# Optimization experiments

Hardware: AMD Instinct MI355X
Metric: run time of the kernel (lower is better)

## Reference

```python
import jax, jax.numpy as jnp
import numpy as np

B, L_IN, D = 4, 4096, 1024
R_MIN, R_MAX = 0.9, 0.999


def setup_inputs() -> dict:
    key = jax.random.key(0)
    k0, k1, k2 = jax.random.split(key, 3)
    inputs = jax.random.normal(k0, (B, L_IN, D), jnp.float32)
    Wi = jax.random.normal(k1, (2 * D, D), jnp.float32) / np.sqrt(D)
    bi = jnp.zeros((2 * D,), jnp.float32)
    Wo = jax.random.normal(k2, (D, 2 * D), jnp.float32) / np.sqrt(2 * D)
    bo = jnp.zeros((D,), jnp.float32)
    # LRU stable-ring initialization, exactly as in the torch module
    rng = np.random.default_rng(0)
    u1 = rng.random(D)
    u2 = rng.random(D)
    v_log = np.log(-0.5 * np.log(u1 * (R_MAX ** 2 - R_MIN ** 2) + R_MIN ** 2))
    theta_log = np.log(u2 * np.pi * 2)
    gamma_log = np.log(np.sqrt(1.0 - np.exp(-np.exp(v_log)) ** 2))
    params_log = jnp.asarray(np.stack([v_log, theta_log, gamma_log]), jnp.float32)
    return {"inputs": inputs, "Wi": Wi, "bi": bi, "Wo": Wo, "bo": bo,
            "params_log": params_log}


def _lru_forward(inputs, Wi, bi, Wo, bo, params_log):
    b, l_in, d = inputs.shape
    u = inputs @ Wi.T + bi                      # [B, L, 2D]
    v, theta, gamma = jnp.exp(params_log)       # each [D]
    # torch.view_as_complex: interleaved (real, imag) pairs along last dim
    uc = u.reshape(b, l_in, d, 2)
    x = jax.lax.complex(uc[..., 0], uc[..., 1])  # [B, L, D] complex64
    log2_L = int(np.ceil(np.log2(l_in)))
    L = 2 ** log2_L
    x = jnp.pad(x, ((0, 0), (0, L - l_in), (0, 0)))
    # Blelloch-style log-depth scan: x_t = lambda * x_{t-1} + u_t,
    # lambda = exp(-v + i*theta)
    for i in range(1, log2_L + 1):
        blk = 2 ** i
        xb = x.reshape(b * L // blk, blk, d)
        x1, x2 = xb[:, : blk // 2], xb[:, blk // 2:]
        pos = jnp.arange(1, blk // 2 + 1, dtype=jnp.float32)  # [blk/2]
        lambs = jnp.exp(jax.lax.complex(-pos[:, None] * v,
                                        pos[:, None] * theta))  # [blk/2, D]
        x2 = x2 + lambs * x1[:, -1:]
        x = jnp.concatenate([x1, x2], axis=1).reshape(b, L, d)
    x = x[:, :l_in] * gamma.astype(x.dtype)     # normalize, drop padding
    xr = jnp.concatenate([x.real, x.imag], axis=-1)  # [B, L, 2D]
    out = xr @ Wo.T + bo
    return jax.nn.relu(out)


def reference(inputs, Wi, bi, Wo, bo, params_log):
    return _lru_forward(inputs, Wi, bi, Wo, bo, params_log)
```

## Files before the change

### kernel.cpp

```cpp
#include <hip/hip_runtime.h>

#define BB 4
#define LL 4096
#define DD 1024
#define SS 64
#define TT 64

typedef __attribute__((ext_vector_type(16))) float  floatx16;
typedef __attribute__((ext_vector_type(8)))  short  shortx8;

static __device__ __forceinline__ unsigned short f2bf(float f) {
    unsigned int u = __float_as_uint(f);
    u += 0x7fffu + ((u >> 16) & 1u);
    return (unsigned short)(u >> 16);
}
static __device__ __forceinline__ float bf2f(unsigned short h) {
    return __uint_as_float(((unsigned int)h) << 16);
}

#define NIN4 (BB * LL * DD / 4)
#define NW4  (2 * DD * DD / 4)
__global__ void cast_all_kernel(const float4* __restrict__ s_in, ushort4* __restrict__ d_inb,
                                const float4* __restrict__ s_wi, ushort4* __restrict__ d_wib,
                                const float4* __restrict__ s_wo, ushort4* __restrict__ d_wob) {
    int i = blockIdx.x * blockDim.x + threadIdx.x;
    const float4* s; ushort4* d; int j;
    if (i < NIN4)                 { s = s_in; d = d_inb; j = i; }
    else if (i < NIN4 + NW4)      { s = s_wi; d = d_wib; j = i - NIN4; }
    else                          { s = s_wo; d = d_wob; j = i - NIN4 - NW4; }
    float4 v = s[j];
    ushort4 o;
    o.x = f2bf(v.x); o.y = f2bf(v.y); o.z = f2bf(v.z); o.w = f2bf(v.w);
    d[j] = o;
}

template<int K, int NT, int EPI>
__global__ __launch_bounds__(256)
void gemm_bt(const unsigned short* __restrict__ A,
             const unsigned short* __restrict__ B,
             const float* __restrict__ bias,
             void* __restrict__ Cp) {
    constexpr int N = NT * 128;
    __shared__ __align__(16) short As[128 * 32];
    __shared__ __align__(16) short Bs[128 * 32];

    const int tid = threadIdx.x;
    const int b   = blockIdx.x;
    const int xcd = b & 7;
    const int i2  = b >> 3;
    const int tileM = ((i2 / NT) * 8 + xcd) * 128;
    const int tileN = (i2 % NT) * 128;

    const int lane = tid & 63;
    const int wave = tid >> 6;
    const int wm   = (wave >> 1) * 64;
    const int wn   = (wave & 1) * 64;
    const int r32  = lane & 31;
    const int ks   = lane >> 5;

    floatx16 acc[2][2] = {};

    const int q0 = tid, q1 = tid + 256;
    const int ra0 = q0 >> 2, ca0 = ((q0 & 3) ^ ((ra0 >> 1) & 3)) * 8;
    const int ra1 = q1 >> 2, ca1 = ((q1 & 3) ^ ((ra1 >> 1) & 3)) * 8;
    short* As0 = &As[(q0 & ~63) * 8];
    short* As1 = &As[(q1 & ~63) * 8];
    short* Bs0 = &Bs[(q0 & ~63) * 8];
    short* Bs1 = &Bs[(q1 & ~63) * 8];

    for (int k0 = 0; k0 < K; k0 += 32) {
        __builtin_amdgcn_global_load_lds(
            (const __attribute__((address_space(1))) void*)&A[(size_t)(tileM + ra0) * K + k0 + ca0],
            (__attribute__((address_space(3))) void*)As0, 16, 0, 0);
        __builtin_amdgcn_global_load_lds(
            (const __attribute__((address_space(1))) void*)&A[(size_t)(tileM + ra1) * K + k0 + ca1],
            (__attribute__((address_space(3))) void*)As1, 16, 0, 0);
        __builtin_amdgcn_global_load_lds(
            (const __attribute__((address_space(1))) void*)&B[(size_t)(tileN + ra0) * K + k0 + ca0],
            (__attribute__((address_space(3))) void*)Bs0, 16, 0, 0);
        __builtin_amdgcn_global_load_lds(
            (const __attribute__((address_space(1))) void*)&B[(size_t)(tileN + ra1) * K + k0 + ca1],
            (__attribute__((address_space(3))) void*)Bs1, 16, 0, 0);
        __syncthreads();

        shortx8 af[2][2], bfr[2][2];
#pragma unroll
        for (int i = 0; i < 2; ++i) {
            const int row = wm + i * 32 + r32;
            const int sw  = (row >> 1) & 3;
#pragma unroll
            for (int kc = 0; kc < 2; ++kc)
                af[i][kc] = *(const shortx8*)(&As[row * 32 + ((kc * 2 + ks) ^ sw) * 8]);
        }
#pragma unroll
        for (int j = 0; j < 2; ++j) {
            const int row = wn + j * 32 + r32;
            const int sw  = (row >> 1) & 3;
#pragma unroll
            for (int kc = 0; kc < 2; ++kc)
                bfr[j][kc] = *(const shortx8*)(&Bs[row * 32 + ((kc * 2 + ks) ^ sw) * 8]);
        }
#pragma unroll
        for (int kc = 0; kc < 2; ++kc)
#pragma unroll
            for (int i = 0; i < 2; ++i)
#pragma unroll
                for (int j = 0; j < 2; ++j)
                    acc[i][j] = __builtin_amdgcn_mfma_f32_32x32x16_bf16(
                        af[i][kc], bfr[j][kc], acc[i][j], 0, 0, 0);
        __syncthreads();
    }

#pragma unroll
    for (int i = 0; i < 2; ++i) {
#pragma unroll
        for (int j = 0; j < 2; ++j) {
            const int col = tileN + wn + j * 32 + r32;
            const float bv = bias[col];
#pragma unroll
            for (int r = 0; r < 16; ++r) {
                const int row = tileM + wm + i * 32 + (r & 3) + 8 * (r >> 2) + 4 * ks;
                float v = acc[i][j][r] + bv;
                if (EPI == 0) {
                    ((unsigned short*)Cp)[(size_t)row * N + col] = f2bf(v);
                } else {
                    ((float*)Cp)[(size_t)row * N + col] = fmaxf(v, 0.0f);
                }
            }
        }
    }
}

__global__ __launch_bounds__(256)
void scanA(const unsigned short* __restrict__ u,
           const float* __restrict__ plog,
           float2* __restrict__ Eend) {
    const int d0 = (blockIdx.x * 256 + threadIdx.x) * 2;
    const int c = blockIdx.y, b = blockIdx.z;
    const float v0  = expf(plog[d0]),      v1  = expf(plog[d0 + 1]);
    const float th0 = expf(plog[DD + d0]), th1 = expf(plog[DD + d0 + 1]);
    const float a0 = expf(-v0), a1 = expf(-v1);
    const float lr0 = a0 * cosf(th0), li0 = a0 * sinf(th0);
    const float lr1 = a1 * cosf(th1), li1 = a1 * sinf(th1);
    float zr0 = 0.f, zi0 = 0.f, zr1 = 0.f, zi1 = 0.f;
    const unsigned short* up = u + (size_t)(b * LL + c * TT) * (2 * DD) + 2 * d0;
#pragma unroll 4
    for (int tl = 0; tl < TT; ++tl) {
        uint2 pr = *(const uint2*)up;
        float xr0 = bf2f((unsigned short)(pr.x & 0xffffu));
        float xi0 = bf2f((unsigned short)(pr.x >> 16));
        float xr1 = bf2f((unsigned short)(pr.y & 0xffffu));
        float xi1 = bf2f((unsigned short)(pr.y >> 16));
        float t;
        t = lr0 * zr0 - li0 * zi0 + xr0; zi0 = lr0 * zi0 + li0 * zr0 + xi0; zr0 = t;
        t = lr1 * zr1 - li1 * zi1 + xr1; zi1 = lr1 * zi1 + li1 * zr1 + xi1; zr1 = t;
        up += 2 * DD;
    }
    *(float4*)&Eend[(size_t)c * (BB * DD) + b * DD + d0] =
        make_float4(zr0, zi0, zr1, zi1);
}

__global__ __launch_bounds__(256)
void scanC(const unsigned short* __restrict__ u,
           const float* __restrict__ plog,
           const float2* __restrict__ Eend,
           unsigned short* __restrict__ xr) {
    const int d0 = (blockIdx.x * 256 + threadIdx.x) * 2;
    const int c = blockIdx.y, b = blockIdx.z;
    const float v0  = expf(plog[d0]),      v1  = expf(plog[d0 + 1]);
    const float th0 = expf(plog[DD + d0]), th1 = expf(plog[DD + d0 + 1]);
    const float g0  = expf(plog[2 * DD + d0]), g1 = expf(plog[2 * DD + d0 + 1]);
    const float a0 = expf(-v0), a1 = expf(-v1);
    const float lr0 = a0 * cosf(th0), li0 = a0 * sinf(th0);
    const float lr1 = a1 * cosf(th1), li1 = a1 * sinf(th1);

    const float aT0 = expf(-(float)TT * v0), aT1 = expf(-(float)TT * v1);
    const float Lr0 = aT0 * cosf((float)TT * th0), Li0 = aT0 * sinf((float)TT * th0);
    const float Lr1 = aT1 * cosf((float)TT * th1), Li1 = aT1 * sinf((float)TT * th1);
    float yr0 = 0.f, yi0 = 0.f, yr1 = 0.f, yi1 = 0.f;
    for (int cc = 0; cc < c; ++cc) {
        float4 e = *(const float4*)&Eend[(size_t)cc * (BB * DD) + b * DD + d0];
        float t;
        t = Lr0 * yr0 - Li0 * yi0 + e.x; yi0 = Lr0 * yi0 + Li0 * yr0 + e.y; yr0 = t;
        t = Lr1 * yr1 - Li1 * yi1 + e.z; yi1 = Lr1 * yi1 + Li1 * yr1 + e.w; yr1 = t;
    }

    const unsigned short* up = u + (size_t)(b * LL + c * TT) * (2 * DD) + 2 * d0;
    unsigned short* xp = xr + (size_t)(b * LL + c * TT) * (2 * DD) + d0;
#pragma unroll 4
    for (int tl = 0; tl < TT; ++tl) {
        uint2 pr = *(const uint2*)up;
        float xr0 = bf2f((unsigned short)(pr.x & 0xffffu));
        float xi0 = bf2f((unsigned short)(pr.x >> 16));
        float xr1 = bf2f((unsigned short)(pr.y & 0xffffu));
        float xi1 = bf2f((unsigned short)(pr.y >> 16));
        float t;
        t = lr0 * yr0 - li0 * yi0 + xr0; yi0 = lr0 * yi0 + li0 * yr0 + xi0; yr0 = t;
        t = lr1 * yr1 - li1 * yi1 + xr1; yi1 = lr1 * yi1 + li1 * yr1 + xi1; yr1 = t;
        *(unsigned int*)&xp[0]  = (unsigned int)f2bf(g0 * yr0) |
                                  ((unsigned int)f2bf(g1 * yr1) << 16);
        *(unsigned int*)&xp[DD] = (unsigned int)f2bf(g0 * yi0) |
                                  ((unsigned int)f2bf(g1 * yi1) << 16);
        up += 2 * DD;
        xp += 2 * DD;
    }
}

extern "C" void kernel_launch(void* const* d_in, const int* in_sizes, int n_in,
                              void* d_out, int out_size, void* d_ws, size_t ws_size,
                              hipStream_t stream) {
    const float* inputs = (const float*)d_in[0];
    const float* Wi     = (const float*)d_in[1];
    const float* bi     = (const float*)d_in[2];
    const float* Wo     = (const float*)d_in[3];
    const float* bo     = (const float*)d_in[4];
    const float* plog   = (const float*)d_in[5];
    float* out = (float*)d_out;

    const size_t M = (size_t)BB * LL;
    unsigned short* u_bf  = (unsigned short*)d_ws;
    unsigned short* xr_bf = u_bf  + M * 2 * DD;
    unsigned short* in_bf = xr_bf + M * 2 * DD;
    unsigned short* Wi_bf = in_bf + M * DD;
    unsigned short* Wo_bf = Wi_bf + (size_t)2 * DD * DD;
    float2* Eend = (float2*)(Wo_bf + (size_t)2 * DD * DD);

    {
        int total4 = NIN4 + 2 * NW4;
        cast_all_kernel<<<total4 / 256, 256, 0, stream>>>(
            (const float4*)inputs, (ushort4*)in_bf,
            (const float4*)Wi,     (ushort4*)Wi_bf,
            (const float4*)Wo,     (ushort4*)Wo_bf);
    }

    gemm_bt<DD, 16, 0><<<(M / 128) * 16, 256, 0, stream>>>(
        in_bf, Wi_bf, bi, (void*)u_bf);

    scanA<<<dim3(DD / 512, SS, BB), 256, 0, stream>>>(u_bf, plog, Eend);
    scanC<<<dim3(DD / 512, SS, BB), 256, 0, stream>>>(u_bf, plog, Eend, xr_bf);

    gemm_bt<2 * DD, 8, 1><<<(M / 128) * 8, 256, 0, stream>>>(
        xr_bf, Wo_bf, bo, (void*)out);
}
```

Before: 353.7 us.

## Switch GEMM to 16x16x32 MFMA with K-step 64 and 8-way swizzled LDS

The bf16 GEMM kernel now stages K=64 per iteration instead of 32, halving the number of barrier pairs per tile, and uses 16x16x32 MFMA instructions on a 4x4 grid of fragments per wave instead of 32x32x16 on a 2x2 grid. The LDS layout uses an 8-chunk XOR swizzle for the wider rows. This aims to cut synchronisation overhead and improve the load-to-compute ratio per step, in exchange for doubled LDS use per block and a different epilogue store pattern.

New measurement: 336.1 us. 5.0% less time.

```diff
diff --git a/kernel.cpp b/kernel.cpp
--- a/kernel.cpp
+++ b/kernel.cpp
@@ -6,8 +6,8 @@
 #define SS 64
 #define TT 64
 
-typedef __attribute__((ext_vector_type(16))) float  floatx16;
-typedef __attribute__((ext_vector_type(8)))  short  shortx8;
+typedef __attribute__((ext_vector_type(4))) float  floatx4;
+typedef __attribute__((ext_vector_type(8))) short  shortx8;
 
 static __device__ __forceinline__ unsigned short f2bf(float f) {
     unsigned int u = __float_as_uint(f);
@@ -41,8 +41,8 @@
              const float* __restrict__ bias,
              void* __restrict__ Cp) {
     constexpr int N = NT * 128;
-    __shared__ __align__(16) short As[128 * 32];
-    __shared__ __align__(16) short Bs[128 * 32];
+    __shared__ __align__(16) short As[128 * 64];
+    __shared__ __align__(16) short Bs[128 * 64];
 
     const int tid = threadIdx.x;
     const int b   = blockIdx.x;
@@ -51,75 +51,67 @@
     const int tileM = ((i2 / NT) * 8 + xcd) * 128;
     const int tileN = (i2 % NT) * 128;
 
-    const int lane = tid & 63;
-    const int wave = tid >> 6;
-    const int wm   = (wave >> 1) * 64;
-    const int wn   = (wave & 1) * 64;
-    const int r32  = lane & 31;
-    const int ks   = lane >> 5;
-
-    floatx16 acc[2][2] = {};
-
-    const int q0 = tid, q1 = tid + 256;
-    const int ra0 = q0 >> 2, ca0 = ((q0 & 3) ^ ((ra0 >> 1) & 3)) * 8;
-    const int ra1 = q1 >> 2, ca1 = ((q1 & 3) ^ ((ra1 >> 1) & 3)) * 8;
-    short* As0 = &As[(q0 & ~63) * 8];
-    short* As1 = &As[(q1 & ~63) * 8];
-    short* Bs0 = &Bs[(q0 & ~63) * 8];
-    short* Bs1 = &Bs[(q1 & ~63) * 8];
-
-    for (int k0 = 0; k0 < K; k0 += 32) {
-        __builtin_amdgcn_global_load_lds(
-            (const __attribute__((address_space(1))) void*)&A[(size_t)(tileM + ra0) * K + k0 + ca0],
-            (__attribute__((address_space(3))) void*)As0, 16, 0, 0);
-        __builtin_amdgcn_global_load_lds(
-            (const __attribute__((address_space(1))) void*)&A[(size_t)(tileM + ra1) * K + k0 + ca1],
-            (__attribute__((address_space(3))) void*)As1, 16, 0, 0);
-        __builtin_amdgcn_global_load_lds(
-            (const __attribute__((address_space(1))) void*)&B[(size_t)(tileN + ra0) * K + k0 + ca0],
-            (__attribute__((address_space(3))) void*)Bs0, 16, 0, 0);
-        __builtin_amdgcn_global_load_lds(
-            (const __attribute__((address_space(1))) void*)&B[(size_t)(tileN + ra1) * K + k0 + ca1],
-            (__attribute__((address_space(3))) void*)Bs1, 16, 0, 0);
+    const int lane  = tid & 63;
+    const int wave  = tid >> 6;
+    const int wm    = (wave >> 1) * 64;
+    const int wn    = (wave & 1) * 64;
+    const int r16   = lane & 15;
+    const int quad  = lane >> 4;
+
+    floatx4 acc[4][4] = {};
+
+    int rowS[4], colS[4];
+#pragma unroll
+    for (int n = 0; n < 4; ++n) {
+        const int q = tid + n * 256;
+        rowS[n] = q >> 3;
+        colS[n] = ((q & 7) ^ (rowS[n] & 7)) * 8;
+    }
+    const int ldsBase = (tid & ~63) * 8;
+
+    const int fx = r16 & 7;
+
+    for (int k0 = 0; k0 < K; k0 += 64) {
+#pragma unroll
+        for (int n = 0; n < 4; ++n) {
+            __builtin_amdgcn_global_load_lds(
+                (const __attribute__((address_space(1))) void*)&A[(size_t)(tileM + rowS[n]) * K + k0 + colS[n]],
+                (__attribute__((address_space(3))) void*)&As[ldsBase + n * 2048], 16, 0, 0);
+            __builtin_amdgcn_global_load_lds(
+                (const __attribute__((address_space(1))) void*)&B[(size_t)(tileN + rowS[n]) * K + k0 + colS[n]],
+                (__attribute__((address_space(3))) void*)&Bs[ldsBase + n * 2048], 16, 0, 0);
+        }
         __syncthreads();
 
-        shortx8 af[2][2], bfr[2][2];
-#pragma unroll
-        for (int i = 0; i < 2; ++i) {
-            const int row = wm + i * 32 + r32;
-            const int sw  = (row >> 1) & 3;
-#pragma unroll
-            for (int kc = 0; kc < 2; ++kc)
-                af[i][kc] = *(const shortx8*)(&As[row * 32 + ((kc * 2 + ks) ^ sw) * 8]);
+#pragma unroll
+        for (int kk = 0; kk < 2; ++kk) {
+            const int slot = ((kk * 4 + quad) ^ fx) * 8;
+            shortx8 af[4], bfv[4];
+#pragma unroll
+            for (int i = 0; i < 4; ++i)
+                af[i] = *(const shortx8*)(&As[(wm + i * 16 + r16) * 64 + slot]);
+#pragma unroll
+            for (int j = 0; j < 4; ++j)
+                bfv[j] = *(const shortx8*)(&Bs[(wn + j * 16 + r16) * 64 + slot]);
+#pragma unroll
+            for (int i = 0; i < 4; ++i)
+#pragma unroll
+                for (int j = 0; j < 4; ++j)
+                    acc[i][j] = __builtin_amdgcn_mfma_f32_16x16x32_bf16(
+                        af[i], bfv[j], acc[i][j], 0, 0, 0);
         }
-#pragma unroll
-        for (int j = 0; j < 2; ++j) {
-            const int row = wn + j * 32 + r32;
-            const int sw  = (row >> 1) & 3;
-#pragma unroll
-            for (int kc = 0; kc < 2; ++kc)
-                bfr[j][kc] = *(const shortx8*)(&Bs[row * 32 + ((kc * 2 + ks) ^ sw) * 8]);
-        }
-#pragma unroll
-        for (int kc = 0; kc < 2; ++kc)
-#pragma unroll
-            for (int i = 0; i < 2; ++i)
-#pragma unroll
-                for (int j = 0; j < 2; ++j)
-                    acc[i][j] = __builtin_amdgcn_mfma_f32_32x32x16_bf16(
-                        af[i][kc], bfr[j][kc], acc[i][j], 0, 0, 0);
         __syncthreads();
     }
 
 #pragma unroll
-    for (int i = 0; i < 2; ++i) {
-#pragma unroll
-        for (int j = 0; j < 2; ++j) {
-            const int col = tileN + wn + j * 32 + r32;
+    for (int i = 0; i < 4; ++i) {
+#pragma unroll
+        for (int j = 0; j < 4; ++j) {
+            const int col = tileN + wn + j * 16 + r16;
             const float bv = bias[col];
 #pragma unroll
-            for (int r = 0; r < 16; ++r) {
-                const int row = tileM + wm + i * 32 + (r & 3) + 8 * (r >> 2) + 4 * ks;
+            for (int r = 0; r < 4; ++r) {
+                const int row = tileM + wm + i * 16 + quad * 4 + r;
                 float v = acc[i][j][r] + bv;
                 if (EPI == 0) {
                     ((unsigned short*)Cp)[(size_t)row * N + col] = f2bf(v);
```
